# Performance work log

Hardware: AMD Instinct MI355X
Metric: run time of the kernel (lower is better)

Reference implementation:

```python
import jax, jax.numpy as jnp
import numpy as np
from jax import lax

K = 3
STRIDE = 1
PAD = 1
DIL = 1


def _rrsvm(x, s):
    # x: [B, C, H, W], s: [C, K, K]
    B, C, H, W = x.shape
    # im2col: [B, C*K*K, Ho, Wo], channel-major patch ordering -> reshape (C, K*K)
    patches = lax.conv_general_dilated_patches(
        x, (K, K), (STRIDE, STRIDE), [(PAD, PAD), (PAD, PAD)],
        rhs_dilation=(DIL, DIL))
    Ho, Wo = patches.shape[2], patches.shape[3]
    p = patches.reshape(B, C, K * K, Ho, Wo)
    # descending sort of each window's values (rank pooling order)
    order = jnp.argsort(-p, axis=2)                      # [B, C, K*K, Ho, Wo]
    sorted_p = jnp.take_along_axis(p, order, axis=2)
    # learned per-rank weights, per channel
    out = jnp.einsum('bckhw,ck->bchw', sorted_p, s.reshape(C, K * K))
    indices = jnp.transpose(order, (0, 1, 3, 4, 2))      # [B, C, Ho, Wo, K*K]
    return out, indices


def setup_inputs() -> dict:
    key = jax.random.key(0)
    k1, k2 = jax.random.split(key)
    B, C, H, W = 16, 128, 56, 56
    x = jax.random.normal(k1, (B, C, H, W), dtype=jnp.float32)
    # module inits s to 1/(C*K*K); use random positive weights for a non-degenerate test
    s = jax.random.uniform(k2, (C, K, K), dtype=jnp.float32) / (K * K)
    return {"x": x, "s": s}


def reference(x, s):
    return _rrsvm(x, s)
```

## Files before the change

kernel.cpp:

```cpp
#include <hip/hip_runtime.h>


#define B_ 16
#define C_ 128
#define H_ 56
#define W_ 56
#define NPIX (B_*C_*H_*W_)
#define BLK 256
#define PXT 4
#define PXB (BLK * PXT)

typedef float v4f __attribute__((ext_vector_type(4)));

__device__ __forceinline__ void sort9(float v[9], float id[9]) {
    #pragma unroll
    for (int rnd = 0; rnd < 9; ++rnd) {
        #pragma unroll
        for (int i = (rnd & 1); i + 1 < 9; i += 2) {
            float vi = v[i], vj = v[i + 1];
            float ii = id[i], ij = id[i + 1];
            bool sw = vj > vi;
            v[i]      = sw ? vj : vi;  v[i + 1]  = sw ? vi : vj;
            id[i]     = sw ? ij : ii;  id[i + 1] = sw ? ii : ij;
        }
    }
}

__global__ __launch_bounds__(BLK) void rrsvm_kernel(
    const float* __restrict__ x, const float* __restrict__ s,
    float* __restrict__ out, float* __restrict__ idxout)
{
    __shared__ float lds[PXB * 9];

    const int tid  = threadIdx.x;
    const int gtid = blockIdx.x * BLK + tid;
    const int pix0 = gtid * PXT;
    const int w0   = pix0 % W_;
    const int t    = pix0 / W_;
    const int h    = t % H_;
    const int bc   = t / H_;
    const int c    = bc & (C_ - 1);

    const float* sp = s + c * 9;
    float sw9[9];
    #pragma unroll
    for (int r = 0; r < 9; ++r) sw9[r] = sp[r];

    const float* img = x + (size_t)bc * (H_ * W_);
    const int r0 = (h > 0)      ? h - 1 : 0;
    const int r2 = (h < H_ - 1) ? h + 1 : H_ - 1;
    const int cl = (w0 > 0)        ? w0 - 1 : 0;
    const int cr = (w0 < W_ - PXT) ? w0 + 4 : W_ - 1;
    const float* p0 = img + r0 * W_;
    const float* p1 = img + h  * W_;
    const float* p2 = img + r2 * W_;

    float T[3][6];
    {
        v4f m0 = *(const v4f*)(p0 + w0);
        v4f m1 = *(const v4f*)(p1 + w0);
        v4f m2 = *(const v4f*)(p2 + w0);
        T[0][0] = p0[cl]; T[0][1] = m0.x; T[0][2] = m0.y; T[0][3] = m0.z; T[0][4] = m0.w; T[0][5] = p0[cr];
        T[1][0] = p1[cl]; T[1][1] = m1.x; T[1][2] = m1.y; T[1][3] = m1.z; T[1][4] = m1.w; T[1][5] = p1[cr];
        T[2][0] = p2[cl]; T[2][1] = m2.x; T[2][2] = m2.y; T[2][3] = m2.z; T[2][4] = m2.w; T[2][5] = p2[cr];
    }

    const bool rv0 = (h > 0), rv2 = (h < H_ - 1);
    const bool cvL = (w0 > 0), cvR = (w0 < W_ - PXT);
    #pragma unroll
    for (int j = 0; j < 6; ++j) {
        T[0][j] = rv0 ? T[0][j] : 0.0f;
        T[2][j] = rv2 ? T[2][j] : 0.0f;
    }
    T[0][0] = cvL ? T[0][0] : 0.0f;
    T[1][0] = cvL ? T[1][0] : 0.0f;
    T[2][0] = cvL ? T[2][0] : 0.0f;
    T[0][5] = cvR ? T[0][5] : 0.0f;
    T[1][5] = cvR ? T[1][5] : 0.0f;
    T[2][5] = cvR ? T[2][5] : 0.0f;

    v4f q[9];
    float oacc[4];
    #pragma unroll
    for (int j = 0; j < PXT; ++j) {
        float v[9]  = { T[0][j], T[0][j+1], T[0][j+2],
                        T[1][j], T[1][j+1], T[1][j+2],
                        T[2][j], T[2][j+1], T[2][j+2] };
        float id[9] = { 0, 1, 2, 3, 4, 5, 6, 7, 8 };
        sort9(v, id);
        float acc = 0.0f;
        #pragma unroll
        for (int r = 0; r < 9; ++r) acc = fmaf(v[r], sw9[r], acc);
        oacc[j] = acc;
        #pragma unroll
        for (int r = 0; r < 9; ++r) {
            const int f = j * 9 + r;
            q[f >> 2][f & 3] = id[r];
        }
    }
    v4f o; o.x = oacc[0]; o.y = oacc[1]; o.z = oacc[2]; o.w = oacc[3];

    __builtin_nontemporal_store(o, (v4f*)(out + pix0));

    v4f* lw = (v4f*)(lds + (size_t)tid * 36);
    #pragma unroll
    for (int k = 0; k < 9; ++k)
        lw[k] = q[k];

    __syncthreads();

    v4f* dst = (v4f*)(idxout + (size_t)blockIdx.x * (PXB * 9));
    const v4f* src = (const v4f*)lds;
    #pragma unroll
    for (int k = 0; k < 9; ++k)
        __builtin_nontemporal_store(src[tid + k * 256], dst + tid + k * 256);
}

extern "C" void kernel_launch(void* const* d_in, const int* in_sizes, int n_in,
                              void* d_out, int out_size, void* d_ws, size_t ws_size,
                              hipStream_t stream) {
    const float* x = (const float*)d_in[0];
    const float* s = (const float*)d_in[1];
    float* out    = (float*)d_out;
    float* idxout = out + NPIX;

    const int nblocks = NPIX / PXB;
    rrsvm_kernel<<<nblocks, BLK, 0, stream>>>(x, s, out, idxout);
}
```

Baseline: 291.1 us.

## Replace odd-even sort with rank counting and byte-packed LDS index staging

Swaps the 9-round odd-even transposition sort, which moved both values and indices, for a rank-by-comparison scheme (36 compares per window) that scatters each tap index into LDS at its computed rank. Indices are staged as bytes and converted to float only at store time, which cuts LDS footprint to a quarter. Per-channel weights are loaded once per block into LDS and read by rank. The cost is dynamic-indexed LDS byte scatters and gathers, and an extra block barrier, in exchange for less ALU work and lower register pressure. Ties resolve by lower tap index first, which should match a stable descending argsort.

```diff
diff --git a/kernel.cpp b/kernel.cpp
--- a/kernel.cpp
+++ b/kernel.cpp
@@ -5,48 +5,40 @@
 #define C_ 128
 #define H_ 56
 #define W_ 56
+#define HW (H_*W_)
 #define NPIX (B_*C_*H_*W_)
 #define BLK 256
 #define PXT 4
 #define PXB (BLK * PXT)
+#define GRID (NPIX / PXB)
 
 typedef float v4f __attribute__((ext_vector_type(4)));
-
-__device__ __forceinline__ void sort9(float v[9], float id[9]) {
-    #pragma unroll
-    for (int rnd = 0; rnd < 9; ++rnd) {
-        #pragma unroll
-        for (int i = (rnd & 1); i + 1 < 9; i += 2) {
-            float vi = v[i], vj = v[i + 1];
-            float ii = id[i], ij = id[i + 1];
-            bool sw = vj > vi;
-            v[i]      = sw ? vj : vi;  v[i + 1]  = sw ? vi : vj;
-            id[i]     = sw ? ij : ii;  id[i + 1] = sw ? ii : ij;
-        }
-    }
-}
 
 __global__ __launch_bounds__(BLK) void rrsvm_kernel(
     const float* __restrict__ x, const float* __restrict__ s,
     float* __restrict__ out, float* __restrict__ idxout)
 {
-    __shared__ float lds[PXB * 9];
+    __shared__ unsigned char lds_idx[PXB * 9];
+    __shared__ float lds_s[24];
 
     const int tid  = threadIdx.x;
-    const int gtid = blockIdx.x * BLK + tid;
-    const int pix0 = gtid * PXT;
+    const int pixr = blockIdx.x * PXB;
+    const int pix0 = pixr + tid * PXT;
     const int w0   = pix0 % W_;
     const int t    = pix0 / W_;
     const int h    = t % H_;
     const int bc   = t / H_;
-    const int c    = bc & (C_ - 1);
 
-    const float* sp = s + c * 9;
-    float sw9[9];
-    #pragma unroll
-    for (int r = 0; r < 9; ++r) sw9[r] = sp[r];
+    const int bcf = pixr / HW;
+    const int bcl = (pixr + PXB - 1) / HW;
+    if (tid < 18) {
+        const int which = (tid >= 9);
+        const int bcx   = which ? bcl : bcf;
+        lds_s[tid] = s[(bcx & (C_ - 1)) * 9 + tid - which * 9];
+    }
+    const int sbase = (bc == bcf) ? 0 : 9;
 
-    const float* img = x + (size_t)bc * (H_ * W_);
+    const float* img = x + (size_t)bc * HW;
     const int r0 = (h > 0)      ? h - 1 : 0;
     const int r2 = (h < H_ - 1) ? h + 1 : H_ - 1;
     const int cl = (w0 > 0)        ? w0 - 1 : 0;
@@ -64,7 +56,6 @@
         T[1][0] = p1[cl]; T[1][1] = m1.x; T[1][2] = m1.y; T[1][3] = m1.z; T[1][4] = m1.w; T[1][5] = p1[cr];
         T[2][0] = p2[cl]; T[2][1] = m2.x; T[2][2] = m2.y; T[2][3] = m2.z; T[2][4] = m2.w; T[2][5] = p2[cr];
     }
-
     const bool rv0 = (h > 0), rv2 = (h < H_ - 1);
     const bool cvL = (w0 > 0), cvR = (w0 < W_ - PXT);
     #pragma unroll
@@ -79,41 +70,51 @@
     T[1][5] = cvR ? T[1][5] : 0.0f;
     T[2][5] = cvR ? T[2][5] : 0.0f;
 
-    v4f q[9];
-    float oacc[4];
+    __syncthreads();
+
+    float oacc[PXT];
     #pragma unroll
-    for (int j = 0; j < PXT; ++j) {
-        float v[9]  = { T[0][j], T[0][j+1], T[0][j+2],
-                        T[1][j], T[1][j+1], T[1][j+2],
-                        T[2][j], T[2][j+1], T[2][j+2] };
-        float id[9] = { 0, 1, 2, 3, 4, 5, 6, 7, 8 };
-        sort9(v, id);
+    for (int px = 0; px < PXT; ++px) {
+        const float v[9] = { T[0][px], T[0][px+1], T[0][px+2],
+                             T[1][px], T[1][px+1], T[1][px+2],
+                             T[2][px], T[2][px+1], T[2][px+2] };
+        int rank[9];
+        #pragma unroll
+        for (int k = 0; k < 9; ++k) rank[k] = 8 - k;
+        #pragma unroll
+        for (int a = 0; a < 8; ++a)
+            #pragma unroll
+            for (int b = a + 1; b < 9; ++b) {
+                const int g = (v[a] >= v[b]);
+                rank[b] += g;
+                rank[a] -= g;
+            }
+        const int base_b = tid * 36 + px * 9;
         float acc = 0.0f;
         #pragma unroll
-        for (int r = 0; r < 9; ++r) acc = fmaf(v[r], sw9[r], acc);
-        oacc[j] = acc;
-        #pragma unroll
-        for (int r = 0; r < 9; ++r) {
-            const int f = j * 9 + r;
-            q[f >> 2][f & 3] = id[r];
+        for (int k = 0; k < 9; ++k) {
+            lds_idx[base_b + rank[k]] = (unsigned char)k;
+            acc = fmaf(v[k], lds_s[sbase + rank[k]], acc);
         }
+        oacc[px] = acc;
     }
     v4f o; o.x = oacc[0]; o.y = oacc[1]; o.z = oacc[2]; o.w = oacc[3];
-
     __builtin_nontemporal_store(o, (v4f*)(out + pix0));
-
-    v4f* lw = (v4f*)(lds + (size_t)tid * 36);
-    #pragma unroll
-    for (int k = 0; k < 9; ++k)
-        lw[k] = q[k];
 
     __syncthreads();
 
-    v4f* dst = (v4f*)(idxout + (size_t)blockIdx.x * (PXB * 9));
-    const v4f* src = (const v4f*)lds;
+    const unsigned int* lu = (const unsigned int*)lds_idx;
+    v4f* dst = (v4f*)(idxout + (size_t)pixr * 9);
     #pragma unroll
-    for (int k = 0; k < 9; ++k)
-        __builtin_nontemporal_store(src[tid + k * 256], dst + tid + k * 256);
+    for (int k = 0; k < 9; ++k) {
+        const unsigned int u = lu[tid + 256 * k];
+        v4f f;
+        f.x = (float)( u        & 0xff);
+        f.y = (float)((u >>  8) & 0xff);
+        f.z = (float)((u >> 16) & 0xff);
+        f.w = (float)((u >> 24)       );
+        __builtin_nontemporal_store(f, dst + tid + 256 * k);
+    }
 }
 
 extern "C" void kernel_launch(void* const* d_in, const int* in_sizes, int n_in,
@@ -124,6 +125,5 @@
     float* out    = (float*)d_out;
     float* idxout = out + NPIX;
 
-    const int nblocks = NPIX / PXB;
-    rrsvm_kernel<<<nblocks, BLK, 0, stream>>>(x, s, out, idxout);
+    rrsvm_kernel<<<GRID, BLK, 0, stream>>>(x, s, out, idxout);
 }
```

After: 271.0 us. 6.9% less time.
